# Performance work log

Hardware: AMD Instinct MI355X
Metric: run time of the kernel (lower is better)

## Reference

```python
import jax, jax.numpy as jnp
import numpy as np

B, S, H, E, V, T = 512, 140, 512, 256, 1000, 21  # T = day_walk_max + 1
PAD, SOS = 0, 2
NDAYS, DLEN = 7, 20


def setup_inputs() -> dict:
    key = jax.random.key(0)
    ks = jax.random.split(key, 16)
    s = 0.05
    return {
        "encoder_hidden": jax.random.normal(ks[0], (1, B, H), jnp.float32),
        "encoder_outputs": jax.random.normal(ks[1], (B, S, H), jnp.float32),
        "label": jax.random.randint(ks[2], (B, T + 1), 0, V),
        "numpairs": jax.random.randint(ks[3], (B, S), 0, 10),
        "emb": jax.random.normal(ks[4], (V, E), jnp.float32) * s,
        "W_ih": jax.random.normal(ks[5], (3 * H, E), jnp.float32) * s,
        "W_hh": jax.random.normal(ks[6], (3 * H, H), jnp.float32) * s,
        "b_ih": jnp.zeros((3 * H,), jnp.float32),
        "b_hh": jnp.zeros((3 * H,), jnp.float32),
        "attn_Wa": jax.random.normal(ks[7], (H, H), jnp.float32) * s,
        "wa_W": jax.random.normal(ks[8], (H, 2 * H), jnp.float32) * s,
        "fc_W": jax.random.normal(ks[9], (V, H), jnp.float32) * s,
        "fc_b": jnp.zeros((V,), jnp.float32),
    }


def _decode(encoder_hidden, encoder_outputs, label, numpairs,
            emb, W_ih, W_hh, b_ih, b_hh, attn_Wa, wa_W, fc_W, fc_b):
    # Luong 'general' attention over 7 day-segments of 20 steps each.
    enc_days = encoder_outputs.reshape(B, NDAYS, DLEN, H)
    mask_day = numpairs.reshape(B, NDAYS, DLEN) != PAD
    # energy is hidden-independent: precompute once  [B,7,20,H]
    energy_day = jnp.einsum('bdsh,gh->bdsg', enc_days, attn_Wa)

    def step(carry, lab_t):
        dec_in, h = carry  # dec_in [B] int, h [B,H]
        # per-day additive attention with numpair padding mask
        sc = jnp.einsum('bh,bdsh->bds', h, energy_day)
        sc = jnp.where(mask_day, sc, jnp.float32(-1e9))
        wd = jax.nn.softmax(sc, axis=-1)
        week = jnp.einsum('bds,bdsh->bdh', wd, enc_days)  # [B,7,H]
        # GRU cell (PyTorch gate layout r,z,n); dropout is identity at eval
        x = emb[dec_in]  # [B,E]
        gi = x @ W_ih.T + b_ih
        gh = h @ W_hh.T + b_hh
        i_r, i_z, i_n = jnp.split(gi, 3, axis=-1)
        h_r, h_z, h_n = jnp.split(gh, 3, axis=-1)
        r = jax.nn.sigmoid(i_r + h_r)
        z = jax.nn.sigmoid(i_z + h_z)
        n = jnp.tanh(i_n + r * h_n)
        h_new = (1.0 - z) * n + z * h  # [B,H]
        # week-level attention over the 7 day contexts (no mask)
        ew = jnp.einsum('bdh,gh->bdg', week, attn_Wa)
        aw = jax.nn.softmax(jnp.einsum('bh,bdh->bd', h_new, ew), axis=-1)
        ctx = jnp.einsum('bd,bdh->bh', aw, week)
        concat = jnp.concatenate([h_new, ctx], axis=-1)  # [B,2H]
        out = jax.nn.log_softmax(jnp.tanh(concat @ wa_W.T) @ fc_W.T + fc_b, axis=-1)
        return (lab_t, h_new), out  # teacher forcing: next input = label[:, t]

    dec0 = jnp.full((B,), SOS, dtype=label.dtype)
    h0 = encoder_hidden[0]  # [B,H]
    labels_t = label[:, :T].T  # [T,B]
    (last_in, _), outs = jax.lax.scan(step, (dec0, h0), labels_t)
    decoder_outputs = jnp.transpose(outs, (1, 0, 2))  # [B,T,V]
    return decoder_outputs, last_in[:, None]


def reference(encoder_hidden, encoder_outputs, label, numpairs,
              emb, W_ih, W_hh, b_ih, b_hh, attn_Wa, wa_W, fc_W, fc_b):
    return _decode(encoder_hidden, encoder_outputs, label, numpairs,
                   emb, W_ih, W_hh, b_ih, b_hh, attn_Wa, wa_W, fc_W, fc_b)
```

## Files before the change

### kernel.cpp

```cpp
#include <hip/hip_runtime.h>
#include <math.h>

typedef __attribute__((ext_vector_type(8))) short bf16x8;
typedef __attribute__((ext_vector_type(4))) float f32x4;

constexpr int NB = 512;
constexpr int NS = 140;
constexpr int NH = 512;
constexpr int NE = 256;
constexpr int NV = 1000;
constexpr int NVP = 1024;
constexpr int NT = 21;
constexpr int ND = 7;
constexpr int DL = 20;
constexpr int SOS = 2;
constexpr int LSTR = NT + 1;
constexpr int NROW = NT * NB;

__device__ __forceinline__ unsigned short f2bf(float f) {
  union { float f; unsigned u; } v; v.f = f;
  unsigned r = v.u + 0x7fffu + ((v.u >> 16) & 1u);
  return (unsigned short)(r >> 16);
}
__device__ __forceinline__ float bf2f(unsigned short h) {
  union { unsigned u; float f; } v; v.u = ((unsigned)h) << 16;
  return v.f;
}
__device__ __forceinline__ void unp8(uint4 v, float* o) {
  o[0] = bf2f((unsigned short)(v.x & 0xffffu)); o[1] = bf2f((unsigned short)(v.x >> 16));
  o[2] = bf2f((unsigned short)(v.y & 0xffffu)); o[3] = bf2f((unsigned short)(v.y >> 16));
  o[4] = bf2f((unsigned short)(v.z & 0xffffu)); o[5] = bf2f((unsigned short)(v.z >> 16));
  o[6] = bf2f((unsigned short)(v.w & 0xffffu)); o[7] = bf2f((unsigned short)(v.w >> 16));
}
__device__ __forceinline__ void unp4(uint2 v, float* o) {
  o[0] = bf2f((unsigned short)(v.x & 0xffffu)); o[1] = bf2f((unsigned short)(v.x >> 16));
  o[2] = bf2f((unsigned short)(v.y & 0xffffu)); o[3] = bf2f((unsigned short)(v.y >> 16));
}

template<int A16, int EPI, int OUT16>
__device__ __forceinline__ void gemm_body(
    const float* __restrict__ Af, const unsigned short* __restrict__ Ah,
    const unsigned short* __restrict__ Bt, const float* __restrict__ bias,
    float* __restrict__ C, unsigned short* __restrict__ C16,
    int K, int lda, int ldc, int bx, int by,
    unsigned short* As, unsigned short* Bs)
{
  const int tid = threadIdx.x;
  const int rowBase = by * 64, colBase = bx * 64;
  const int wave = tid >> 6, lane = tid & 63, quad = lane >> 4, l15 = lane & 15;
  const int rw = (wave & 1) * 32, cw = (wave >> 1) * 32;

  f32x4 acc[2][2];
#pragma unroll
  for (int i = 0; i < 2; ++i)
#pragma unroll
    for (int j = 0; j < 2; ++j)
#pragma unroll
      for (int r = 0; r < 4; ++r) acc[i][j][r] = 0.f;

  const int ar = tid >> 2;
  const int kq = (tid & 3) * 8;
  const float* aptrf = nullptr;
  const unsigned short* aptrh = nullptr;
  if (A16) aptrh = Ah + (size_t)(rowBase + ar) * lda + kq;
  else     aptrf = Af + (size_t)(rowBase + ar) * lda + kq;
  const unsigned short* bptr = Bt + (size_t)(colBase + ar) * K + kq;
  unsigned short* asd = &As[ar * 40 + kq];
  unsigned short* bsd = &Bs[ar * 40 + kq];

  float4 x0, x1;
  uint4 av;
  if (A16) {
    av = *(const uint4*)aptrh;
  } else {
    x0 = *(const float4*)aptrf; x1 = *(const float4*)(aptrf + 4);
  }
  uint4 bv = *(const uint4*)bptr;

  int cur = 0;
  for (int k0 = 0; k0 < K; k0 += 32) {
    uint4 aw;
    if (A16) {
      aw = av;
    } else {
      aw.x = (unsigned)f2bf(x0.x) | ((unsigned)f2bf(x0.y) << 16);
      aw.y = (unsigned)f2bf(x0.z) | ((unsigned)f2bf(x0.w) << 16);
      aw.z = (unsigned)f2bf(x1.x) | ((unsigned)f2bf(x1.y) << 16);
      aw.w = (unsigned)f2bf(x1.z) | ((unsigned)f2bf(x1.w) << 16);
    }
    *(uint4*)(asd + cur * 2560) = aw;
    *(uint4*)(bsd + cur * 2560) = bv;

    const int kn = k0 + 32;
    if (kn < K) {
      if (A16) {
        av = *(const uint4*)(aptrh + kn);
      } else {
        x0 = *(const float4*)(aptrf + kn);
        x1 = *(const float4*)(aptrf + kn + 4);
      }
      bv = *(const uint4*)(bptr + kn);
    }
    __syncthreads();

    const unsigned short* Ab = As + cur * 2560;
    const unsigned short* Bb = Bs + cur * 2560;
    const bf16x8 af0 = *(const bf16x8*)&Ab[(rw + l15) * 40 + quad * 8];
    const bf16x8 af1 = *(const bf16x8*)&Ab[(rw + 16 + l15) * 40 + quad * 8];
    const bf16x8 bf0 = *(const bf16x8*)&Bb[(cw + l15) * 40 + quad * 8];
    const bf16x8 bf1 = *(const bf16x8*)&Bb[(cw + 16 + l15) * 40 + quad * 8];
    acc[0][0] = __builtin_amdgcn_mfma_f32_16x16x32_bf16(af0, bf0, acc[0][0], 0, 0, 0);
    acc[0][1] = __builtin_amdgcn_mfma_f32_16x16x32_bf16(af0, bf1, acc[0][1], 0, 0, 0);
    acc[1][0] = __builtin_amdgcn_mfma_f32_16x16x32_bf16(af1, bf0, acc[1][0], 0, 0, 0);
    acc[1][1] = __builtin_amdgcn_mfma_f32_16x16x32_bf16(af1, bf1, acc[1][1], 0, 0, 0);
    cur ^= 1;
  }

#pragma unroll
  for (int i = 0; i < 2; ++i) {
    const int grow = rowBase + rw + 16 * i + quad * 4;
#pragma unroll
    for (int j = 0; j < 2; ++j) {
      const int gcol = colBase + cw + 16 * j + l15;
#pragma unroll
      for (int r = 0; r < 4; ++r) {
        float vo = acc[i][j][r];
        if (EPI == 1) vo += (gcol < NV) ? bias[gcol] : 0.f;
        if (EPI == 2) vo = tanhf(vo);
        if (OUT16) C16[(size_t)(grow + r) * ldc + gcol] = f2bf(vo);
        else       C[(size_t)(grow + r) * ldc + gcol] = vo;
      }
    }
  }
}

template<int A16, int EPI, int OUT16>
__global__ __launch_bounds__(256) void gemm_k(
    const float* __restrict__ Af, const unsigned short* __restrict__ Ah,
    const unsigned short* __restrict__ Bt, const float* __restrict__ bias,
    float* __restrict__ C, unsigned short* __restrict__ C16,
    int K, int lda, int ldc)
{
  __shared__ unsigned short As[2 * 64 * 40];
  __shared__ unsigned short Bs[2 * 64 * 40];
  gemm_body<A16, EPI, OUT16>(Af, Ah, Bt, bias, C, C16, K, lda, ldc,
                             blockIdx.x, blockIdx.y, As, Bs);
}

__global__ __launch_bounds__(256) void gemm_gather(
    const float* __restrict__ emb, const unsigned short* __restrict__ Wiht,
    unsigned short* __restrict__ Gi, const int* __restrict__ label)
{
  __shared__ unsigned short As[64 * 40];
  __shared__ unsigned short Bs[64 * 40];
  const int tid = threadIdx.x;
  const int rowBase = blockIdx.y * 64, colBase = blockIdx.x * 64;
  const int wave = tid >> 6, lane = tid & 63, quad = lane >> 4, l15 = lane & 15;
  const int rw = (wave & 1) * 32, cw = (wave >> 1) * 32;
  const int K = 256;

  f32x4 acc[2][2];
#pragma unroll
  for (int i = 0; i < 2; ++i)
#pragma unroll
    for (int j = 0; j < 2; ++j)
#pragma unroll
      for (int r = 0; r < 4; ++r) acc[i][j][r] = 0.f;

  const int ar = tid >> 2;
  const int kq = (tid & 3) * 8;
  const int aRowG = rowBase + ar;
  const int t = aRowG >> 9;
  const int b = aRowG & 511;
  const int dec = (t == 0) ? SOS : label[b * LSTR + (t - 1)];
  const float* aptr = emb + (size_t)dec * NE + kq;
  const unsigned short* bptr = Wiht + (size_t)(colBase + ar) * K + kq;
  unsigned short* asd = &As[ar * 40 + kq];
  unsigned short* bsd = &Bs[ar * 40 + kq];

  float4 x0 = *(const float4*)aptr;
  float4 x1 = *(const float4*)(aptr + 4);
  uint4 bv = *(const uint4*)bptr;

  for (int k0 = 0; k0 < K; k0 += 32) {
    uint4 aw;
    aw.x = (unsigned)f2bf(x0.x) | ((unsigned)f2bf(x0.y) << 16);
    aw.y = (unsigned)f2bf(x0.z) | ((unsigned)f2bf(x0.w) << 16);
    aw.z = (unsigned)f2bf(x1.x) | ((unsigned)f2bf(x1.y) << 16);
    aw.w = (unsigned)f2bf(x1.z) | ((unsigned)f2bf(x1.w) << 16);
    *(uint4*)asd = aw;
    *(uint4*)bsd = bv;
    __syncthreads();
    const int kn = k0 + 32;
    if (kn < K) {
      x0 = *(const float4*)(aptr + kn);
      x1 = *(const float4*)(aptr + kn + 4);
      bv = *(const uint4*)(bptr + kn);
    }
    const bf16x8 af0 = *(const bf16x8*)&As[(rw + l15) * 40 + quad * 8];
    const bf16x8 af1 = *(const bf16x8*)&As[(rw + 16 + l15) * 40 + quad * 8];
    const bf16x8 bf0 = *(const bf16x8*)&Bs[(cw + l15) * 40 + quad * 8];
    const bf16x8 bf1 = *(const bf16x8*)&Bs[(cw + 16 + l15) * 40 + quad * 8];
    acc[0][0] = __builtin_amdgcn_mfma_f32_16x16x32_bf16(af0, bf0, acc[0][0], 0, 0, 0);
    acc[0][1] = __builtin_amdgcn_mfma_f32_16x16x32_bf16(af0, bf1, acc[0][1], 0, 0, 0);
    acc[1][0] = __builtin_amdgcn_mfma_f32_16x16x32_bf16(af1, bf0, acc[1][0], 0, 0, 0);
    acc[1][1] = __builtin_amdgcn_mfma_f32_16x16x32_bf16(af1, bf1, acc[1][1], 0, 0, 0);
    __syncthreads();
  }

#pragma unroll
  for (int i = 0; i < 2; ++i) {
    const int grow = rowBase + rw + 16 * i + quad * 4;
#pragma unroll
    for (int j = 0; j < 2; ++j) {
      const int gcol = colBase + cw + 16 * j + l15;
#pragma unroll
      for (int r = 0; r < 4; ++r)
        Gi[(size_t)(grow + r) * 1536 + gcol] = f2bf(acc[i][j][r]);
    }
  }
}

__global__ __launch_bounds__(256) void step_fused(
    const float* __restrict__ Ht, const unsigned short* __restrict__ W2,
    const unsigned short* __restrict__ Gi_t,
    const float* __restrict__ b_ih, const float* __restrict__ b_hh,
    float* __restrict__ Hnext, float* __restrict__ Ut,
    unsigned short* __restrict__ U16t, int notLast)
{
  __shared__ __align__(16) char smem[25600];
  unsigned short* As = (unsigned short*)smem;
  unsigned short* Bs = (unsigned short*)(smem + 5120);
  float* Gbuf = (float*)smem;

  const int tid = threadIdx.x;
  const int wave = tid >> 6, lane = tid & 63, quad = lane >> 4, l15 = lane & 15;
  const int rowBase = blockIdx.y * 32;
  const int G = blockIdx.x;

  f32x4 acc[2][2];
#pragma unroll
  for (int i = 0; i < 2; ++i)
#pragma unroll
    for (int j = 0; j < 2; ++j)
#pragma unroll
      for (int r = 0; r < 4; ++r) acc[i][j][r] = 0.f;

  const int ar = tid >> 3;
  const int kqa = (tid & 7) * 4;
  const float* aptr = Ht + (size_t)(rowBase + ar) * NH + kqa;
  const unsigned short* bsrc = W2 + (size_t)(G * 128) * 32 + (tid >> 1) * 32 + (tid & 1) * 16;
  unsigned short* asd = As + ar * 40 + kqa;
  unsigned short* bdst = Bs + (tid >> 1) * 40 + (tid & 1) * 16;

  float4 xa = *(const float4*)aptr;
  uint4 b0 = ((const uint4*)bsrc)[0];
  uint4 b1 = ((const uint4*)bsrc)[1];

  int cur = 0;
  for (int c = 0; c < 16; ++c) {
    ushort4 aw;
    aw.x = f2bf(xa.x); aw.y = f2bf(xa.y); aw.z = f2bf(xa.z); aw.w = f2bf(xa.w);
    *(ushort4*)(asd + cur * 1280) = aw;
    *(uint4*)(bdst + cur * 5120) = b0;
    *(uint4*)(bdst + cur * 5120 + 8) = b1;

    const int cn = c + 1;
    if (cn < 16) {
      xa = *(const float4*)(aptr + cn * 32);
      const unsigned short* nb = bsrc + (size_t)cn * (2048 * 32);
      b0 = ((const uint4*)nb)[0];
      b1 = ((const uint4*)nb)[1];
    }
    __syncthreads();

    const unsigned short* Ab = As + cur * 1280;
    const unsigned short* Bb = Bs + cur * 5120;
    const bf16x8 af0 = *(const bf16x8*)&Ab[(l15) * 40 + quad * 8];
    const bf16x8 af1 = *(const bf16x8*)&Ab[(16 + l15) * 40 + quad * 8];
#pragma unroll
    for (int j = 0; j < 2; ++j) {
      const bf16x8 bf = *(const bf16x8*)&Bb[(wave * 32 + j * 16 + l15) * 40 + quad * 8];
      acc[0][j] = __builtin_amdgcn_mfma_f32_16x16x32_bf16(af0, bf, acc[0][j], 0, 0, 0);
      acc[1][j] = __builtin_amdgcn_mfma_f32_16x16x32_bf16(af1, bf, acc[1][j], 0, 0, 0);
    }
    cur ^= 1;
  }
  __syncthreads();

#pragma unroll
  for (int i = 0; i < 2; ++i) {
#pragma unroll
    for (int j = 0; j < 2; ++j) {
#pragma unroll
      for (int r = 0; r < 4; ++r) {
        const int rl = 16 * i + quad * 4 + r;
        const int jj = j * 16 + l15;
        const float v = acc[i][j][r];
        if (wave == 3) {
          const size_t off = (size_t)(rowBase + rl) * NH + G * 32 + jj;
          Ut[off] = v;
          U16t[off] = f2bf(v);
        } else {
          Gbuf[(wave * 32 + rl) * 40 + jj] = v;
        }
      }
    }
  }
  __syncthreads();

  if (notLast) {
    const int rl = tid >> 3, c4 = (tid & 7) * 4;
    const int bg = rowBase + rl;
    const int j0 = G * 32 + c4;
    const float4 g0 = *(const float4*)(Gbuf + (0 * 32 + rl) * 40 + c4);
    const float4 g1 = *(const float4*)(Gbuf + (1 * 32 + rl) * 40 + c4);
    const float4 g2 = *(const float4*)(Gbuf + (2 * 32 + rl) * 40 + c4);
    const unsigned short* gp = Gi_t + (size_t)bg * 1536;
    float gr[4], gz[4], gn[4];
    { uint2 a = *(const uint2*)(gp + j0);        unp4(a, gr); }
    { uint2 a = *(const uint2*)(gp + 512 + j0);  unp4(a, gz); }
    { uint2 a = *(const uint2*)(gp + 1024 + j0); unp4(a, gn); }
    const float4 bi0 = *(const float4*)(b_ih + j0);
    const float4 bi1 = *(const float4*)(b_ih + 512 + j0);
    const float4 bi2 = *(const float4*)(b_ih + 1024 + j0);
    const float4 bh0 = *(const float4*)(b_hh + j0);
    const float4 bh1 = *(const float4*)(b_hh + 512 + j0);
    const float4 bh2 = *(const float4*)(b_hh + 1024 + j0);
    const float4 ho = *(const float4*)(Ht + (size_t)bg * NH + j0);
    const float ghr[4] = {g0.x, g0.y, g0.z, g0.w};
    const float ghz[4] = {g1.x, g1.y, g1.z, g1.w};
    const float ghn[4] = {g2.x, g2.y, g2.z, g2.w};
    const float bi0a[4] = {bi0.x, bi0.y, bi0.z, bi0.w};
    const float bi1a[4] = {bi1.x, bi1.y, bi1.z, bi1.w};
    const float bi2a[4] = {bi2.x, bi2.y, bi2.z, bi2.w};
    const float bh0a[4] = {bh0.x, bh0.y, bh0.z, bh0.w};
    const float bh1a[4] = {bh1.x, bh1.y, bh1.z, bh1.w};
    const float bh2a[4] = {bh2.x, bh2.y, bh2.z, bh2.w};
    const float hov[4] = {ho.x, ho.y, ho.z, ho.w};
    float o[4];
#pragma unroll
    for (int c = 0; c < 4; ++c) {
      const float rg = 1.f / (1.f + expf(-(gr[c] + bi0a[c] + ghr[c] + bh0a[c])));
      const float zg = 1.f / (1.f + expf(-(gz[c] + bi1a[c] + ghz[c] + bh1a[c])));
      const float ng = tanhf(gn[c] + bi2a[c] + rg * (ghn[c] + bh2a[c]));
      o[c] = (1.f - zg) * ng + zg * hov[c];
    }
    *(float4*)(Hnext + (size_t)bg * NH + j0) = make_float4(o[0], o[1], o[2], o[3]);
  }
}

__global__ __launch_bounds__(256) void day_attn_mfma(
    const float* __restrict__ enc, const int* __restrict__ numpairs,
    const unsigned short* __restrict__ U16, unsigned short* __restrict__ week)
{
  __shared__ __align__(16) char smem[46016];
  unsigned short* Erow = (unsigned short*)smem;
  unsigned short* ETs  = (unsigned short*)(smem + 20800);
  float*          S_lds = (float*)(smem + 39232);
  unsigned short* P_lds = (unsigned short*)(smem + 43456);

  const int tid = threadIdx.x;
  const int wave = tid >> 6, lane = tid & 63;
  const int quad = lane >> 4, l15 = lane & 15;
  const int b = blockIdx.x / ND, d = blockIdx.x % ND;
  const int mt = wave >> 1, nt = wave & 1;

  for (int i = tid; i < 256 * 6; i += 256)
    *(unsigned*)&ETs[(i / 6) * 36 + 20 + (i % 6) * 2] = 0;
  for (int i = tid; i < 640; i += 256) ((unsigned*)P_lds)[i] = 0;

  const float* eb = enc + ((size_t)b * NS + d * DL) * NH;
  for (int f = tid; f < DL * NH / 4; f += 256) {
    const int s = f >> 7, h = (f & 127) * 4;
    const float4 v = *(const float4*)(eb + s * NH + h);
    ushort4 hs;
    hs.x = f2bf(v.x); hs.y = f2bf(v.y); hs.z = f2bf(v.z); hs.w = f2bf(v.w);
    *(ushort4*)&Erow[s * 520 + h] = hs;
  }

  bf16x8 qa[16];
  {
    const int m = mt * 16 + l15;
    const int t = (m < NT + 1) ? m : NT;
    const unsigned short* qp = U16 + ((size_t)t * NB + b) * NH + quad * 8;
#pragma unroll
    for (int ks = 0; ks < 16; ++ks)
      qa[ks] = *(const bf16x8*)(qp + ks * 32);
  }
  __syncthreads();

  for (int i = tid; i < 32 * DL; i += 256) {
    const int s = i % DL, h8 = i / DL;
    const uint4 v = *(const uint4*)&Erow[s * 520 + h8 * 8];
    const unsigned short* u = (const unsigned short*)&v;
#pragma unroll
    for (int c = 0; c < 8; ++c)
      ETs[(h8 * 8 + c) * 36 + s] = u[c];
  }

  f32x4 sacc = {0.f, 0.f, 0.f, 0.f};
#pragma unroll
  for (int ks = 0; ks < 16; ++ks) {
    const bf16x8 bf = *(const bf16x8*)&Erow[(nt * 16 + l15) * 520 + ks * 32 + quad * 8];
    sacc = __builtin_amdgcn_mfma_f32_16x16x32_bf16(qa[ks], bf, sacc, 0, 0, 0);
  }
#pragma unroll
  for (int r = 0; r < 4; ++r)
    S_lds[(mt * 16 + quad * 4 + r) * 33 + nt * 16 + l15] = sacc[r];
  __syncthreads();

  {
    const int r = tid >> 3, c = tid & 7;
    const int base = b * NS + d * DL;
    float v0 = S_lds[r * 33 + c];
    if (numpairs[base + c] == 0) v0 = -1e9f;
    float v1 = S_lds[r * 33 + c + 8];
    if (numpairs[base + c + 8] == 0) v1 = -1e9f;
    float v2 = -1e30f;
    if (c < 4) {
      v2 = S_lds[r * 33 + c + 16];
      if (numpairs[base + c + 16] == 0) v2 = -1e9f;
    }
    float mx = fmaxf(fmaxf(v0, v1), v2);
    mx = fmaxf(mx, __shfl_xor(mx, 1));
    mx = fmaxf(mx, __shfl_xor(mx, 2));
    mx = fmaxf(mx, __shfl_xor(mx, 4));
    const float e0 = expf(v0 - mx), e1 = expf(v1 - mx);
    const float e2 = (c < 4) ? expf(v2 - mx) : 0.f;
    float sm = e0 + e1 + e2;
    sm += __shfl_xor(sm, 1);
    sm += __shfl_xor(sm, 2);
    sm += __shfl_xor(sm, 4);
    const float inv = 1.f / sm;
    P_lds[r * 40 + c] = f2bf(e0 * inv);
    P_lds[r * 40 + c + 8] = f2bf(e1 * inv);
    if (c < 4) P_lds[r * 40 + c + 16] = f2bf(e2 * inv);
  }
  __syncthreads();

  const bf16x8 pa = *(const bf16x8*)&P_lds[(mt * 16 + l15) * 40 + quad * 8];
#pragma unroll
  for (int p = 0; p < 2; ++p) {
    if (p == 1) {
      for (int i = tid; i < 32 * DL; i += 256) {
        const int s = i % DL, h8 = i / DL;
        const uint4 v = *(const uint4*)&Erow[s * 520 + 256 + h8 * 8];
        const unsigned short* u = (const unsigned short*)&v;
#pragma unroll
        for (int c = 0; c < 8; ++c)
          ETs[(h8 * 8 + c) * 36 + s] = u[c];
      }
      __syncthreads();
    }
#pragma unroll
    for (int j = 0; j < 8; ++j) {
      const int hl = nt * 128 + j * 16;
      const bf16x8 bf = *(const bf16x8*)&ETs[(hl + l15) * 36 + quad * 8];
      f32x4 oacc = {0.f, 0.f, 0.f, 0.f};
      oacc = __builtin_amdgcn_mfma_f32_16x16x32_bf16(pa, bf, oacc, 0, 0, 0);
#pragma unroll
      for (int r = 0; r < 4; ++r) {
        const int t = mt * 16 + quad * 4 + r;
        if (t < NT)
          week[(((size_t)t * NB + b) * ND + d) * NH + p * 256 + hl + l15] = f2bf(oacc[r]);
      }
    }
    if (p == 0) __syncthreads();
  }
}

__global__ __launch_bounds__(256) void wk_ctx(
    const float* __restrict__ U, const unsigned short* __restrict__ week,
    const float* __restrict__ H, unsigned short* __restrict__ concat)
{
  __shared__ float scS[16 * ND];
  __shared__ float awS[16 * ND];
  const int tid = threadIdx.x;
  const int t = blockIdx.x >> 5;
  const int grp = blockIdx.x & 31;
  const int b16 = tid >> 4, k16 = tid & 15;
  const int b = grp * 16 + b16;
  const float* vp = U + ((size_t)(t + 1) * NB + b) * NH + k16 * 32;
  const size_t wrow = ((size_t)t * NB + b) * ND;

  for (int d = 0; d < ND; ++d) {
    const unsigned short* wp = week + (wrow + d) * NH + k16 * 32;
    float p = 0.f;
#pragma unroll
    for (int q = 0; q < 8; ++q) {
      const float4 a = *(const float4*)(vp + q * 4);
      const ushort4 wv = *(const ushort4*)(wp + q * 4);
      p += a.x * bf2f(wv.x) + a.y * bf2f(wv.y) + a.z * bf2f(wv.z) + a.w * bf2f(wv.w);
    }
    p += __shfl_down(p, 8); p += __shfl_down(p, 4);
    p += __shfl_down(p, 2); p += __shfl_down(p, 1);
    if (k16 == 0) scS[b16 * ND + d] = p;
  }
  __syncthreads();
  if (tid < 16) {
    float s[ND], mx = -1e30f;
    for (int d = 0; d < ND; ++d) { s[d] = scS[tid * ND + d]; mx = fmaxf(mx, s[d]); }
    float sum = 0.f;
    for (int d = 0; d < ND; ++d) { float e = expf(s[d] - mx); s[d] = e; sum += e; }
    const float inv = 1.f / sum;
    for (int d = 0; d < ND; ++d) awS[tid * ND + d] = s[d] * inv;
  }
  __syncthreads();

  const int c0 = k16 * 32;
  const float* hp = H + ((size_t)(t + 1) * NB + b) * NH + c0;
  float aw[ND];
#pragma unroll
  for (int d = 0; d < ND; ++d) aw[d] = awS[b16 * ND + d];
  unsigned short* crow = concat + ((size_t)t * NB + b) * 1024;
#pragma unroll
  for (int q = 0; q < 8; ++q) {
    const int c = c0 + q * 4;
    const float4 hv = *(const float4*)(hp + q * 4);
    ushort4 hs;
    hs.x = f2bf(hv.x); hs.y = f2bf(hv.y); hs.z = f2bf(hv.z); hs.w = f2bf(hv.w);
    *(ushort4*)(crow + c) = hs;
    float4 cv = make_float4(0.f, 0.f, 0.f, 0.f);
#pragma unroll
    for (int d = 0; d < ND; ++d) {
      const ushort4 wv = *(const ushort4*)(week + (wrow + d) * NH + c);
      cv.x += aw[d] * bf2f(wv.x); cv.y += aw[d] * bf2f(wv.y);
      cv.z += aw[d] * bf2f(wv.z); cv.w += aw[d] * bf2f(wv.w);
    }
    ushort4 cs;
    cs.x = f2bf(cv.x); cs.y = f2bf(cv.y); cs.z = f2bf(cv.z); cs.w = f2bf(cv.w);
    *(ushort4*)(crow + 512 + c) = cs;
  }
}

__global__ __launch_bounds__(256) void lsm_k(
    const float* __restrict__ logits, float* __restrict__ out)
{
  __shared__ float red[8];
  const int tid = threadIdx.x;
  const int wave = tid >> 6, lane = tid & 63;
  const int r = blockIdx.x;
  const int t = r >> 9, b = r & (NB - 1);
  const float* row = logits + (size_t)r * NVP;
  float v[4];
  float mx = -1e30f;
#pragma unroll
  for (int k = 0; k < 4; ++k) {
    const int c = tid + k * 256;
    v[k] = row[c];
    if (c < NV) mx = fmaxf(mx, v[k]);
  }
#pragma unroll
  for (int off = 32; off; off >>= 1) mx = fmaxf(mx, __shfl_xor(mx, off));
  if (lane == 0) red[wave] = mx;
  __syncthreads();
  mx = fmaxf(fmaxf(red[0], red[1]), fmaxf(red[2], red[3]));
  float s = 0.f;
#pragma unroll
  for (int k = 0; k < 4; ++k) {
    const int c = tid + k * 256;
    if (c < NV) s += expf(v[k] - mx);
  }
#pragma unroll
  for (int off = 32; off; off >>= 1) s += __shfl_xor(s, off);
  if (lane == 0) red[4 + wave] = s;
  __syncthreads();
  const float lse = mx + logf(red[4] + red[5] + red[6] + red[7]);
  float* orow = out + ((size_t)b * NT + t) * NV;
#pragma unroll
  for (int k = 0; k < 4; ++k) {
    const int c = tid + k * 256;
    if (c < NV) orow[c] = v[k] - lse;
  }
}

__global__ void write_last(const int* __restrict__ label, float* __restrict__ out2)
{
  const int b = blockIdx.x * 256 + threadIdx.x;
  if (b < NB) out2[b] = (float)label[b * LSTR + (NT - 1)];
}

__global__ __launch_bounds__(256) void pack_w2(
    const float* __restrict__ Whh, const float* __restrict__ Wa,
    unsigned short* __restrict__ W2)
{
  const int idx = blockIdx.x * 256 + threadIdx.x;
  const int np = idx >> 9, k = idx & 511;
  const int G = np >> 7, rem = np & 127, gate = rem >> 5, j = G * 32 + (rem & 31);
  float v;
  if (gate < 3) v = Whh[(size_t)(gate * 512 + j) * 512 + k];
  else          v = Wa[(size_t)k * 512 + j];
  W2[((size_t)(k >> 5) * 2048 + np) * 32 + (k & 31)] = f2bf(v);
}

__global__ __launch_bounds__(256) void cast4(
    const float4* __restrict__ in, ushort4* __restrict__ out, int n4)
{
  const int i = blockIdx.x * 256 + threadIdx.x;
  if (i < n4) {
    const float4 x = in[i];
    ushort4 r;
    r.x = f2bf(x.x); r.y = f2bf(x.y); r.z = f2bf(x.z); r.w = f2bf(x.w);
    out[i] = r;
  }
}

extern "C" void kernel_launch(void* const* d_in, const int* in_sizes, int n_in,
                              void* d_out, int out_size, void* d_ws, size_t ws_size,
                              hipStream_t stream)
{
  const float* enc_h  = (const float*)d_in[0];
  const float* enc    = (const float*)d_in[1];
  const int*   label  = (const int*)d_in[2];
  const int*   numprs = (const int*)d_in[3];
  const float* emb    = (const float*)d_in[4];
  const float* W_ih   = (const float*)d_in[5];
  const float* W_hh   = (const float*)d_in[6];
  const float* b_ih   = (const float*)d_in[7];
  const float* b_hh   = (const float*)d_in[8];
  const float* Wa     = (const float*)d_in[9];
  const float* wa_W   = (const float*)d_in[10];
  const float* fc_W   = (const float*)d_in[11];
  const float* fc_b   = (const float*)d_in[12];
  float* out = (float*)d_out;

  float* f = (float*)d_ws;
  float* H_all   = f; f += (size_t)(NT + 1) * NB * NH;
  float* U_all   = f; f += (size_t)(NT + 1) * NB * NH;
  float* logitsW = f; f += (size_t)NROW * NVP;
  unsigned short* us = (unsigned short*)f;
  unsigned short* U16    = us; us += (size_t)(NT + 1) * NB * NH;
  unsigned short* W2     = us; us += (size_t)2048 * 512;
  unsigned short* W3t    = us; us += (size_t)512 * 1024;
  unsigned short* W4t    = us; us += (size_t)NVP * 512;
  unsigned short* Wiht   = us; us += (size_t)1536 * 256;
  unsigned short* Gi     = us; us += (size_t)NT * NB * 1536;
  unsigned short* week   = us; us += (size_t)NT * NB * ND * NH;
  unsigned short* concatW= us; us += (size_t)NROW * 1024;
  unsigned short* aBuf   = us; us += (size_t)NROW * 512;

  const dim3 blk(256);
  const size_t BH = (size_t)NB * NH;

  hipMemcpyAsync(H_all, enc_h, BH * sizeof(float),
                 hipMemcpyDeviceToDevice, stream);

  pack_w2<<<dim3(2048 * 512 / 256), blk, 0, stream>>>(W_hh, Wa, W2);
  cast4<<<dim3(512 * 1024 / 4 / 256), blk, 0, stream>>>(
      (const float4*)wa_W, (ushort4*)W3t, 512 * 1024 / 4);
  cast4<<<dim3((NV * 512 / 4 + 255) / 256), blk, 0, stream>>>(
      (const float4*)fc_W, (ushort4*)W4t, NV * 512 / 4);
  hipMemsetAsync(W4t + (size_t)NV * 512, 0, (size_t)(NVP - NV) * 512 * 2, stream);
  cast4<<<dim3(1536 * 256 / 4 / 256), blk, 0, stream>>>(
      (const float4*)W_ih, (ushort4*)Wiht, 1536 * 256 / 4);
  gemm_gather<<<dim3(24, NT * 8), blk, 0, stream>>>(emb, Wiht, Gi, label);

  for (int t = 0; t <= NT; ++t) {
    const int notLast = (t < NT) ? 1 : 0;
    const int tg = (t < NT) ? t : NT - 1;
    step_fused<<<dim3(16, 16), blk, 0, stream>>>(
        H_all + (size_t)t * BH, W2, Gi + (size_t)tg * NB * 1536,
        b_ih, b_hh,
        H_all + (size_t)(notLast ? t + 1 : t) * BH,
        U_all + (size_t)t * BH, U16 + (size_t)t * BH, notLast);
  }

  day_attn_mfma<<<dim3(NB * ND), blk, 0, stream>>>(enc, numprs, U16, week);
  wk_ctx<<<dim3(NT * 32), blk, 0, stream>>>(U_all, week, H_all, concatW);
  gemm_k<1, 2, 1><<<dim3(8, NROW / 64), blk, 0, stream>>>(
      nullptr, concatW, W3t, nullptr, nullptr, aBuf, 1024, 1024, 512);
  gemm_k<1, 1, 0><<<dim3(16, NROW / 64), blk, 0, stream>>>(
      nullptr, aBuf, W4t, fc_b, logitsW, nullptr, 512, 512, NVP);
  lsm_k<<<dim3(NROW), blk, 0, stream>>>(logitsW, out);
  write_last<<<dim3(2), blk, 0, stream>>>(label, out + (size_t)NB * NT * NV);
}
```

Before: 675.0 us.

## Halve step tile width, double grid, stage hidden state in bf16, relayout U16

The recurrent step kernel now gives each block 16 output columns per gate instead of 32, which doubles the grid from 256 to 512 blocks, and uses a K chunk of 64 instead of 32. The W2 packing is changed to match the new tiling. Each step also writes a bf16 copy of the next hidden state into ping-pong buffers, so the next step loads bf16 directly instead of converting fp32 in its load loop. U16 is relaid out as batch-major with time inside, which changes how day attention reads the queries. The aim is better occupancy and fewer conversions on the serial 22-launch recurrence, at the cost of less B-tile reuse per block and an extra bf16 store per step.

```diff
diff --git a/kernel.cpp b/kernel.cpp
--- a/kernel.cpp
+++ b/kernel.cpp
@@ -16,6 +16,7 @@
 constexpr int SOS = 2;
 constexpr int LSTR = NT + 1;
 constexpr int NROW = NT * NB;
+constexpr int UST = LSTR * NH;
 
 __device__ __forceinline__ unsigned short f2bf(float f) {
   union { float f; unsigned u; } v; v.f = f;
@@ -26,15 +27,9 @@
   union { unsigned u; float f; } v; v.u = ((unsigned)h) << 16;
   return v.f;
 }
-__device__ __forceinline__ void unp8(uint4 v, float* o) {
-  o[0] = bf2f((unsigned short)(v.x & 0xffffu)); o[1] = bf2f((unsigned short)(v.x >> 16));
-  o[2] = bf2f((unsigned short)(v.y & 0xffffu)); o[3] = bf2f((unsigned short)(v.y >> 16));
-  o[4] = bf2f((unsigned short)(v.z & 0xffffu)); o[5] = bf2f((unsigned short)(v.z >> 16));
-  o[6] = bf2f((unsigned short)(v.w & 0xffffu)); o[7] = bf2f((unsigned short)(v.w >> 16));
-}
-__device__ __forceinline__ void unp4(uint2 v, float* o) {
-  o[0] = bf2f((unsigned short)(v.x & 0xffffu)); o[1] = bf2f((unsigned short)(v.x >> 16));
-  o[2] = bf2f((unsigned short)(v.y & 0xffffu)); o[3] = bf2f((unsigned short)(v.y >> 16));
+__device__ __forceinline__ void unp2(unsigned v, float* o) {
+  o[0] = bf2f((unsigned short)(v & 0xffffu));
+  o[1] = bf2f((unsigned short)(v >> 16));
 }
 
 template<int A16, int EPI, int OUT16>
@@ -222,67 +217,66 @@
 }
 
 __global__ __launch_bounds__(256) void step_fused(
-    const float* __restrict__ Ht, const unsigned short* __restrict__ W2,
+    const float* __restrict__ Ht, const unsigned short* __restrict__ Ht16,
+    const unsigned short* __restrict__ W2,
     const unsigned short* __restrict__ Gi_t,
     const float* __restrict__ b_ih, const float* __restrict__ b_hh,
-    float* __restrict__ Hnext, float* __restrict__ Ut,
-    unsigned short* __restrict__ U16t, int notLast)
-{
-  __shared__ __align__(16) char smem[25600];
+    float* __restrict__ Hnext, unsigned short* __restrict__ H16next,
+    float* __restrict__ Ut, unsigned short* __restrict__ U16,
+    int tIdx, int notLast)
+{
+  __shared__ __align__(16) char smem[27648];
   unsigned short* As = (unsigned short*)smem;
-  unsigned short* Bs = (unsigned short*)(smem + 5120);
+  unsigned short* Bs = (unsigned short*)(smem + 9216);
   float* Gbuf = (float*)smem;
 
   const int tid = threadIdx.x;
   const int wave = tid >> 6, lane = tid & 63, quad = lane >> 4, l15 = lane & 15;
   const int rowBase = blockIdx.y * 32;
   const int G = blockIdx.x;
-
-  f32x4 acc[2][2];
+  const int j0 = G * 16;
+
+  f32x4 acc[2];
 #pragma unroll
   for (int i = 0; i < 2; ++i)
 #pragma unroll
-    for (int j = 0; j < 2; ++j)
-#pragma unroll
-      for (int r = 0; r < 4; ++r) acc[i][j][r] = 0.f;
-
-  const int ar = tid >> 3;
-  const int kqa = (tid & 7) * 4;
-  const float* aptr = Ht + (size_t)(rowBase + ar) * NH + kqa;
-  const unsigned short* bsrc = W2 + (size_t)(G * 128) * 32 + (tid >> 1) * 32 + (tid & 1) * 16;
-  unsigned short* asd = As + ar * 40 + kqa;
-  unsigned short* bdst = Bs + (tid >> 1) * 40 + (tid & 1) * 16;
-
-  float4 xa = *(const float4*)aptr;
-  uint4 b0 = ((const uint4*)bsrc)[0];
-  uint4 b1 = ((const uint4*)bsrc)[1];
+    for (int r = 0; r < 4; ++r) acc[i][r] = 0.f;
+
+  const int arow = tid >> 3, ak = (tid & 7) * 8;
+  const unsigned short* aptr = Ht16 + (size_t)(rowBase + arow) * NH + ak;
+  unsigned short* asd = As + arow * 72 + ak;
+  const int bn = tid >> 2, bk = (tid & 3) * 16;
+  const unsigned short* bptr = W2 + ((size_t)(G * 64 + bn)) * 64 + bk;
+  unsigned short* bsd = Bs + bn * 72 + bk;
+
+  uint4 av = *(const uint4*)aptr;
+  uint4 bv0 = ((const uint4*)bptr)[0];
+  uint4 bv1 = ((const uint4*)bptr)[1];
 
   int cur = 0;
-  for (int c = 0; c < 16; ++c) {
-    ushort4 aw;
-    aw.x = f2bf(xa.x); aw.y = f2bf(xa.y); aw.z = f2bf(xa.z); aw.w = f2bf(xa.w);
-    *(ushort4*)(asd + cur * 1280) = aw;
-    *(uint4*)(bdst + cur * 5120) = b0;
-    *(uint4*)(bdst + cur * 5120 + 8) = b1;
+  for (int c = 0; c < 8; ++c) {
+    *(uint4*)(asd + cur * 2304) = av;
+    *(uint4*)(bsd + cur * 4608) = bv0;
+    *(uint4*)(bsd + cur * 4608 + 8) = bv1;
 
     const int cn = c + 1;
-    if (cn < 16) {
-      xa = *(const float4*)(aptr + cn * 32);
-      const unsigned short* nb = bsrc + (size_t)cn * (2048 * 32);
-      b0 = ((const uint4*)nb)[0];
-      b1 = ((const uint4*)nb)[1];
+    if (cn < 8) {
+      av = *(const uint4*)(aptr + cn * 64);
+      const unsigned short* nb = bptr + (size_t)cn * (2048 * 64);
+      bv0 = ((const uint4*)nb)[0];
+      bv1 = ((const uint4*)nb)[1];
     }
     __syncthreads();
 
-    const unsigned short* Ab = As + cur * 1280;
-    const unsigned short* Bb = Bs + cur * 5120;
-    const bf16x8 af0 = *(const bf16x8*)&Ab[(l15) * 40 + quad * 8];
-    const bf16x8 af1 = *(const bf16x8*)&Ab[(16 + l15) * 40 + quad * 8];
-#pragma unroll
-    for (int j = 0; j < 2; ++j) {
-      const bf16x8 bf = *(const bf16x8*)&Bb[(wave * 32 + j * 16 + l15) * 40 + quad * 8];
-      acc[0][j] = __builtin_amdgcn_mfma_f32_16x16x32_bf16(af0, bf, acc[0][j], 0, 0, 0);
-      acc[1][j] = __builtin_amdgcn_mfma_f32_16x16x32_bf16(af1, bf, acc[1][j], 0, 0, 0);
+    const unsigned short* Ab = As + cur * 2304;
+    const unsigned short* Bb = Bs + cur * 4608;
+#pragma unroll
+    for (int s = 0; s < 2; ++s) {
+      const bf16x8 af0 = *(const bf16x8*)&Ab[(l15) * 72 + s * 32 + quad * 8];
+      const bf16x8 af1 = *(const bf16x8*)&Ab[(16 + l15) * 72 + s * 32 + quad * 8];
+      const bf16x8 bf = *(const bf16x8*)&Bb[(wave * 16 + l15) * 72 + s * 32 + quad * 8];
+      acc[0] = __builtin_amdgcn_mfma_f32_16x16x32_bf16(af0, bf, acc[0], 0, 0, 0);
+      acc[1] = __builtin_amdgcn_mfma_f32_16x16x32_bf16(af1, bf, acc[1], 0, 0, 0);
     }
     cur ^= 1;
   }
@@ -291,62 +285,54 @@
 #pragma unroll
   for (int i = 0; i < 2; ++i) {
 #pragma unroll
-    for (int j = 0; j < 2; ++j) {
-#pragma unroll
-      for (int r = 0; r < 4; ++r) {
-        const int rl = 16 * i + quad * 4 + r;
-        const int jj = j * 16 + l15;
-        const float v = acc[i][j][r];
-        if (wave == 3) {
-          const size_t off = (size_t)(rowBase + rl) * NH + G * 32 + jj;
-          Ut[off] = v;
-          U16t[off] = f2bf(v);
-        } else {
-          Gbuf[(wave * 32 + rl) * 40 + jj] = v;
-        }
+    for (int r = 0; r < 4; ++r) {
+      const int rl = 16 * i + quad * 4 + r;
+      const float v = acc[i][r];
+      if (wave == 3) {
+        const int bg = rowBase + rl;
+        Ut[(size_t)bg * NH + j0 + l15] = v;
+        U16[(size_t)bg * UST + tIdx * NH + j0 + l15] = f2bf(v);
+      } else {
+        Gbuf[(wave * 32 + rl) * 20 + l15] = v;
       }
     }
   }
   __syncthreads();
 
   if (notLast) {
-    const int rl = tid >> 3, c4 = (tid & 7) * 4;
+    const int rl = tid >> 3, p2 = (tid & 7) * 2;
     const int bg = rowBase + rl;
-    const int j0 = G * 32 + c4;
-    const float4 g0 = *(const float4*)(Gbuf + (0 * 32 + rl) * 40 + c4);
-    const float4 g1 = *(const float4*)(Gbuf + (1 * 32 + rl) * 40 + c4);
-    const float4 g2 = *(const float4*)(Gbuf + (2 * 32 + rl) * 40 + c4);
+    const int jg = j0 + p2;
+    const float2 g0 = *(const float2*)(Gbuf + (0 * 32 + rl) * 20 + p2);
+    const float2 g1 = *(const float2*)(Gbuf + (1 * 32 + rl) * 20 + p2);
+    const float2 g2 = *(const float2*)(Gbuf + (2 * 32 + rl) * 20 + p2);
     const unsigned short* gp = Gi_t + (size_t)bg * 1536;
-    float gr[4], gz[4], gn[4];
-    { uint2 a = *(const uint2*)(gp + j0);        unp4(a, gr); }
-    { uint2 a = *(const uint2*)(gp + 512 + j0);  unp4(a, gz); }
-    { uint2 a = *(const uint2*)(gp + 1024 + j0); unp4(a, gn); }
-    const float4 bi0 = *(const float4*)(b_ih + j0);
-    const float4 bi1 = *(const float4*)(b_ih + 512 + j0);
-    const float4 bi2 = *(const float4*)(b_ih + 1024 + j0);
-    const float4 bh0 = *(const float4*)(b_hh + j0);
-    const float4 bh1 = *(const float4*)(b_hh + 512 + j0);
-    const float4 bh2 = *(const float4*)(b_hh + 1024 + j0);
-    const float4 ho = *(const float4*)(Ht + (size_t)bg * NH + j0);
-    const float ghr[4] = {g0.x, g0.y, g0.z, g0.w};
-    const float ghz[4] = {g1.x, g1.y, g1.z, g1.w};
-    const float ghn[4] = {g2.x, g2.y, g2.z, g2.w};
-    const float bi0a[4] = {bi0.x, bi0.y, bi0.z, bi0.w};
-    const float bi1a[4] = {bi1.x, bi1.y, bi1.z, bi1.w};
-    const float bi2a[4] = {bi2.x, bi2.y, bi2.z, bi2.w};
-    const float bh0a[4] = {bh0.x, bh0.y, bh0.z, bh0.w};
-    const float bh1a[4] = {bh1.x, bh1.y, bh1.z, bh1.w};
-    const float bh2a[4] = {bh2.x, bh2.y, bh2.z, bh2.w};
-    const float hov[4] = {ho.x, ho.y, ho.z, ho.w};
-    float o[4];
-#pragma unroll
-    for (int c = 0; c < 4; ++c) {
+    float gr[2], gz[2], gn[2];
+    unp2(*(const unsigned*)(gp + jg), gr);
+    unp2(*(const unsigned*)(gp + 512 + jg), gz);
+    unp2(*(const unsigned*)(gp + 1024 + jg), gn);
+    const float2 bi0 = *(const float2*)(b_ih + jg);
+    const float2 bi1 = *(const float2*)(b_ih + 512 + jg);
+    const float2 bi2 = *(const float2*)(b_ih + 1024 + jg);
+    const float2 bh0 = *(const float2*)(b_hh + jg);
+    const float2 bh1 = *(const float2*)(b_hh + 512 + jg);
+    const float2 bh2 = *(const float2*)(b_hh + 1024 + jg);
+    const float2 ho = *(const float2*)(Ht + (size_t)bg * NH + jg);
+    const float ghr[2] = {g0.x, g0.y}, ghz[2] = {g1.x, g1.y}, ghn[2] = {g2.x, g2.y};
+    const float bi0a[2] = {bi0.x, bi0.y}, bi1a[2] = {bi1.x, bi1.y}, bi2a[2] = {bi2.x, bi2.y};
+    const float bh0a[2] = {bh0.x, bh0.y}, bh1a[2] = {bh1.x, bh1.y}, bh2a[2] = {bh2.x, bh2.y};
+    const float hov[2] = {ho.x, ho.y};
+    float o[2];
+#pragma unroll
+    for (int c = 0; c < 2; ++c) {
       const float rg = 1.f / (1.f + expf(-(gr[c] + bi0a[c] + ghr[c] + bh0a[c])));
       const float zg = 1.f / (1.f + expf(-(gz[c] + bi1a[c] + ghz[c] + bh1a[c])));
       const float ng = tanhf(gn[c] + bi2a[c] + rg * (ghn[c] + bh2a[c]));
       o[c] = (1.f - zg) * ng + zg * hov[c];
     }
-    *(float4*)(Hnext + (size_t)bg * NH + j0) = make_float4(o[0], o[1], o[2], o[3]);
+    *(float2*)(Hnext + (size_t)bg * NH + jg) = make_float2(o[0], o[1]);
+    *(unsigned*)(H16next + (size_t)bg * NH + jg) =
+        (unsigned)f2bf(o[0]) | ((unsigned)f2bf(o[1]) << 16);
   }
 }
 
@@ -383,7 +369,7 @@
   {
     const int m = mt * 16 + l15;
     const int t = (m < NT + 1) ? m : NT;
-    const unsigned short* qp = U16 + ((size_t)t * NB + b) * NH + quad * 8;
+    const unsigned short* qp = U16 + (size_t)b * UST + t * NH + quad * 8;
 #pragma unroll
     for (int ks = 0; ks < 16; ++ks)
       qa[ks] = *(const bf16x8*)(qp + ks * 32);
@@ -587,11 +573,11 @@
 {
   const int idx = blockIdx.x * 256 + threadIdx.x;
   const int np = idx >> 9, k = idx & 511;
-  const int G = np >> 7, rem = np & 127, gate = rem >> 5, j = G * 32 + (rem & 31);
+  const int G = np >> 6, rem = np & 63, gate = rem >> 4, j = G * 16 + (rem & 15);
   float v;
   if (gate < 3) v = Whh[(size_t)(gate * 512 + j) * 512 + k];
   else          v = Wa[(size_t)k * 512 + j];
-  W2[((size_t)(k >> 5) * 2048 + np) * 32 + (k & 31)] = f2bf(v);
+  W2[((size_t)(k >> 6) * 2048 + np) * 64 + (k & 63)] = f2bf(v);
 }
 
 __global__ __launch_bounds__(256) void cast4(
@@ -630,7 +616,9 @@
   float* U_all   = f; f += (size_t)(NT + 1) * NB * NH;
   float* logitsW = f; f += (size_t)NROW * NVP;
   unsigned short* us = (unsigned short*)f;
-  unsigned short* U16    = us; us += (size_t)(NT + 1) * NB * NH;
+  unsigned short* U16    = us; us += (size_t)NB * UST;
+  unsigned short* H16a   = us; us += (size_t)NB * NH;
+  unsigned short* H16b   = us; us += (size_t)NB * NH;
   unsigned short* W2     = us; us += (size_t)2048 * 512;
   unsigned short* W3t    = us; us += (size_t)512 * 1024;
   unsigned short* W4t    = us; us += (size_t)NVP * 512;
@@ -639,6 +627,7 @@
   unsigned short* week   = us; us += (size_t)NT * NB * ND * NH;
   unsigned short* concatW= us; us += (size_t)NROW * 1024;
   unsigned short* aBuf   = us; us += (size_t)NROW * 512;
+  unsigned short* H16p[2] = {H16a, H16b};
 
   const dim3 blk(256);
   const size_t BH = (size_t)NB * NH;
@@ -647,6 +636,8 @@
                  hipMemcpyDeviceToDevice, stream);
 
   pack_w2<<<dim3(2048 * 512 / 256), blk, 0, stream>>>(W_hh, Wa, W2);
+  cast4<<<dim3(BH / 4 / 256), blk, 0, stream>>>(
+      (const float4*)enc_h, (ushort4*)H16a, (int)(BH / 4));
   cast4<<<dim3(512 * 1024 / 4 / 256), blk, 0, stream>>>(
       (const float4*)wa_W, (ushort4*)W3t, 512 * 1024 / 4);
   cast4<<<dim3((NV * 512 / 4 + 255) / 256), blk, 0, stream>>>(
@@ -659,11 +650,11 @@
   for (int t = 0; t <= NT; ++t) {
     const int notLast = (t < NT) ? 1 : 0;
     const int tg = (t < NT) ? t : NT - 1;
-    step_fused<<<dim3(16, 16), blk, 0, stream>>>(
-        H_all + (size_t)t * BH, W2, Gi + (size_t)tg * NB * 1536,
-        b_ih, b_hh,
-        H_all + (size_t)(notLast ? t + 1 : t) * BH,
-        U_all + (size_t)t * BH, U16 + (size_t)t * BH, notLast);
+    step_fused<<<dim3(32, 16), blk, 0, stream>>>(
+        H_all + (size_t)t * BH, H16p[t & 1], W2,
+        Gi + (size_t)tg * NB * 1536, b_ih, b_hh,
+        H_all + (size_t)(notLast ? t + 1 : t) * BH, H16p[(t + 1) & 1],
+        U_all + (size_t)t * BH, U16, t, notLast);
   }
 
   day_attn_mfma<<<dim3(NB * ND), blk, 0, stream>>>(enc, numprs, U16, week);
```

Result: faster. 640.6 us (-5.1%).
